# Optimization experiments

Hardware: AMD Instinct MI355X
Metric: run time of the kernel (lower is better)

The kernel has to match this reference:

```python
import jax, jax.numpy as jnp
import numpy as np

B, T = 512, 64
STOCH, DETER, HIDDEN = 30, 200, 200
A, EMBED = 12, 1024
MIN_STD = 0.1
UPDATE_BIAS = -1.0


def _linear_init(key, fan_in, fan_out):
    w_key, b_key = jax.random.split(key)
    lim = 1.0 / np.sqrt(fan_in)
    W = jax.random.uniform(w_key, (fan_in, fan_out), minval=-lim, maxval=lim, dtype=jnp.float32)
    b = jax.random.uniform(b_key, (fan_out,), minval=-lim, maxval=lim, dtype=jnp.float32)
    return W, b


def setup_inputs() -> dict:
    key = jax.random.key(0)
    ks = jax.random.split(key, 12)
    embed = jax.random.normal(ks[0], (B, T, EMBED), dtype=jnp.float32)
    action = jax.random.normal(ks[1], (B, T, A), dtype=jnp.float32)
    noise_prior = jax.random.normal(ks[2], (B, T, STOCH), dtype=jnp.float32)
    noise_post = jax.random.normal(ks[3], (B, T, STOCH), dtype=jnp.float32)
    inp_W, inp_b = _linear_init(ks[4], STOCH + A, HIDDEN)          # _inp_layers
    gru_W, gru_b = _linear_init(ks[5], HIDDEN + DETER, 3 * DETER)  # GRUCell._layer
    img_out_W, img_out_b = _linear_init(ks[6], DETER, HIDDEN)      # _img_out_layers
    ims_W, ims_b = _linear_init(ks[7], HIDDEN, 2 * STOCH)          # _ims_stat_layer
    obs_out_W, obs_out_b = _linear_init(ks[8], DETER + EMBED, HIDDEN)  # _obs_out_layers
    obs_W, obs_b = _linear_init(ks[9], HIDDEN, 2 * STOCH)          # _obs_stat_layer
    return dict(embed=embed, action=action, noise_prior=noise_prior, noise_post=noise_post,
                inp_W=inp_W, inp_b=inp_b, gru_W=gru_W, gru_b=gru_b,
                img_out_W=img_out_W, img_out_b=img_out_b, ims_W=ims_W, ims_b=ims_b,
                obs_out_W=obs_out_W, obs_out_b=obs_out_b, obs_W=obs_W, obs_b=obs_b)


def _observe(embed, action, noise_prior, noise_post,
             inp_W, inp_b, gru_W, gru_b, img_out_W, img_out_b,
             ims_W, ims_b, obs_out_W, obs_out_b, obs_W, obs_b):
    # time-major for scan: [T, B, ...]
    emb_t = jnp.swapaxes(embed, 0, 1)
    act_t = jnp.swapaxes(action, 0, 1)
    npr_t = jnp.swapaxes(noise_prior, 0, 1)
    npo_t = jnp.swapaxes(noise_post, 0, 1)

    def step(carry, xs):
        stoch, deter = carry                    # posterior stoch [B,STOCH], deter [B,DETER]
        a, e, nz_pr, nz_po = xs
        # img_step: input MLP
        x = jax.nn.elu(jnp.concatenate([stoch, a], -1) @ inp_W + inp_b)
        # GRUCell (norm=False)
        parts = jnp.concatenate([x, deter], -1) @ gru_W + gru_b   # [B, 3*DETER]
        reset, cand, update = jnp.split(parts, 3, -1)
        reset = jax.nn.sigmoid(reset)
        cand = jnp.tanh(reset * cand)
        update = jax.nn.sigmoid(update + UPDATE_BIAS)
        deter_new = update * cand + (1.0 - update) * deter
        # prior stats
        h = jax.nn.elu(deter_new @ img_out_W + img_out_b)
        mean_pr, std_pr = jnp.split(h @ ims_W + ims_b, 2, -1)
        std_pr = jax.nn.softplus(std_pr) + MIN_STD
        stoch_pr = mean_pr + std_pr * nz_pr
        # posterior (temp_post=True): cat(deter, embed)
        ho = jax.nn.elu(jnp.concatenate([deter_new, e], -1) @ obs_out_W + obs_out_b)
        mean_po, std_po = jnp.split(ho @ obs_W + obs_b, 2, -1)
        std_po = jax.nn.softplus(std_po) + MIN_STD
        stoch_po = mean_po + std_po * nz_po
        out = (stoch_po, mean_po, std_po, stoch_pr, mean_pr, std_pr, deter_new)
        return (stoch_po, deter_new), out

    init = (jnp.zeros((B, STOCH), jnp.float32), jnp.zeros((B, DETER), jnp.float32))
    _, outs = jax.lax.scan(step, init, (act_t, emb_t, npr_t, npo_t))
    # back to batch-major and pack into a single array [B, T, 6*STOCH + DETER]
    outs = [jnp.swapaxes(o, 0, 1) for o in outs]
    return jnp.concatenate(outs, -1)


def reference(embed, action, noise_prior, noise_post,
              inp_W, inp_b, gru_W, gru_b, img_out_W, img_out_b,
              ims_W, ims_b, obs_out_W, obs_out_b, obs_W, obs_b):
    return _observe(embed, action, noise_prior, noise_post,
                    inp_W, inp_b, gru_W, gru_b, img_out_W, img_out_b,
                    ims_W, ims_b, obs_out_W, obs_out_b, obs_W, obs_b)
```

## Files before the change

### kernel.cpp

```cpp
#include <hip/hip_runtime.h>

typedef _Float16 h2   __attribute__((ext_vector_type(2)));
typedef _Float16 h4   __attribute__((ext_vector_type(4)));
typedef _Float16 half8 __attribute__((ext_vector_type(8)));
typedef float f32x4   __attribute__((ext_vector_type(4)));

#define MFMA16(a,b,c) __builtin_amdgcn_mfma_f32_16x16x32_f16((a),(b),(c),0,0,0)
#define ATOMIC_ST(p,v) __hip_atomic_store((p),(v),__ATOMIC_RELAXED,__HIP_MEMORY_SCOPE_AGENT)
#define ATOMIC_LD(p)   __hip_atomic_load((p),__ATOMIC_RELAXED,__HIP_MEMORY_SCOPE_AGENT)


#define EP_HALVES ((size_t)32768*208)

__global__ void prep_frags(const float* __restrict__ inpW, const float* __restrict__ gruW,
                           const float* __restrict__ imgW, const float* __restrict__ obsoutW,
                           const float* __restrict__ imsW, const float* __restrict__ obsW,
                           _Float16* __restrict__ frags) {
    int gb = blockIdx.x, lane = threadIdx.x;
    const float* src; int KS, K, N, ld, roff = 0, local;
    if (gb < 26)       { src = inpW;    KS = 2;  K = 42;   N = 200; ld = 200; local = gb; }
    else if (gb < 520) { src = gruW;    KS = 13; K = 400;  N = 600; ld = 600; local = gb - 26; }
    else if (gb < 611) { src = imgW;    KS = 7;  K = 200;  N = 200; ld = 200; local = gb - 520; }
    else if (gb < 702) { src = obsoutW; KS = 7;  K = 200;  N = 200; ld = 200; local = gb - 611; }
    else if (gb < 730) { src = imsW;    KS = 7;  K = 200;  N = 60;  ld = 60;  local = gb - 702; }
    else if (gb < 758) { src = obsW;    KS = 7;  K = 200;  N = 60;  ld = 60;  local = gb - 730; }
    else               { src = obsoutW; KS = 32; K = 1024; N = 200; ld = 200; roff = 200; local = gb - 758; }
    int nt = local / KS, ks = local % KS;
    int n  = nt * 16 + (lane & 15);
    int k0 = ks * 32 + (lane >> 4) * 8;
    half8 v;
#pragma unroll
    for (int j = 0; j < 8; ++j) {
        int k = k0 + j;
        float f = (k < K && n < N) ? src[(size_t)(k + roff) * ld + n] : 0.0f;
        v[j] = (_Float16)f;
    }
    *(half8*)(frags + (size_t)gb * 512 + lane * 8) = v;
}

__global__ __launch_bounds__(256) void ep_gemm(const float* __restrict__ embed,
                                               const _Float16* __restrict__ w2f,
                                               _Float16* __restrict__ ep) {
    __shared__ __align__(16) _Float16 aE[16 * 1048];
    int tid = threadIdx.x;
    int rb = blockIdx.x * 16;
#pragma unroll
    for (int i = 0; i < 16; ++i) {
        float4 e = *((const float4*)(embed + (size_t)(rb + i) * 1024) + tid);
        h4 hv; hv[0] = (_Float16)e.x; hv[1] = (_Float16)e.y; hv[2] = (_Float16)e.z; hv[3] = (_Float16)e.w;
        *(h4*)(aE + i * 1048 + tid * 4) = hv;
    }
    __syncthreads();
    int w = tid >> 6, lane = tid & 63, m = lane & 15, q = lane >> 4;
    f32x4 acc[4] = {};
    int nts[4]; int ntc = 0;
    for (int nt = w; nt < 13; nt += 4) nts[ntc++] = nt;
    half8 bb[2][4];
#pragma unroll
    for (int j = 0; j < 4; ++j) if (j < ntc)
        bb[0][j] = *(const half8*)(w2f + ((size_t)(nts[j] * 32) * 64 + lane) * 8);
#pragma unroll
    for (int ks = 0; ks < 32; ++ks) {
        int cur = ks & 1, nxt = cur ^ 1;
        if (ks < 31) {
#pragma unroll
            for (int j = 0; j < 4; ++j) if (j < ntc)
                bb[nxt][j] = *(const half8*)(w2f + ((size_t)(nts[j] * 32 + ks + 1) * 64 + lane) * 8);
        }
        half8 a = *(const half8*)(aE + m * 1048 + ks * 32 + q * 8);
#pragma unroll
        for (int j = 0; j < 4; ++j) if (j < ntc)
            acc[j] = MFMA16(a, bb[cur][j], acc[j]);
    }
    for (int j = 0; j < ntc; ++j) {
        int col = nts[j] * 16 + m;
#pragma unroll
        for (int i = 0; i < 4; ++i)
            ep[(size_t)(rb + q * 4 + i) * 208 + col] = (_Float16)acc[j][i];
    }
}

__device__ __forceinline__ float sigm_(float x) { return 1.0f / (1.0f + __expf(-x)); }
__device__ __forceinline__ float tanh_(float x) { float e = __expf(2.0f * x); return 1.0f - 2.0f / (e + 1.0f); }
__device__ __forceinline__ float elu_(float x)  { return x > 0.0f ? x : __expf(x) - 1.0f; }
__device__ __forceinline__ float sp_(float x)   { return fmaxf(x, 0.0f) + log1pf(__expf(-fabsf(x))); }
__device__ __forceinline__ unsigned packh2(float a, float b) {
    h2 p; p[0] = (_Float16)a; p[1] = (_Float16)b;
    return __builtin_bit_cast(unsigned, p);
}

__global__ __launch_bounds__(512, 2) void rssm_scan(
    const float* __restrict__ action, const float* __restrict__ npr, const float* __restrict__ npo,
    const float* __restrict__ inp_b, const float* __restrict__ gru_b,
    const float* __restrict__ img_b, const float* __restrict__ obsout_b,
    const float* __restrict__ ims_b, const float* __restrict__ obs_b,
    const _Float16* __restrict__ frags, const _Float16* __restrict__ ep,
    unsigned* __restrict__ qdet, unsigned* __restrict__ stochb,
    unsigned* __restrict__ flags, float* __restrict__ out) {

    __shared__ __align__(16) unsigned actI[16 * 36];
    __shared__ __align__(16) unsigned actG[16 * 212];
    __shared__ __align__(16) unsigned actX[16 * 116];
    __shared__ __align__(16) _Float16 parts[16 * 208];
    __shared__ float statspre[16 * 65];
    __shared__ float bias[1320];

    const _Float16* Finp  = frags;
    const _Float16* Fgru  = frags + (size_t)26  * 512;
    const _Float16* Fimg  = frags + (size_t)520 * 512;
    const _Float16* Fobsd = frags + (size_t)611 * 512;
    const _Float16* Fims  = frags + (size_t)702 * 512;
    const _Float16* Fobs  = frags + (size_t)730 * 512;

    const int tid = threadIdx.x, w = tid >> 6, lane = tid & 63, m = lane & 15, q = lane >> 4;
    const int g = blockIdx.x & 31, wg = blockIdx.x >> 5;
    const int rb = g * 16;
    const bool post = (wg >= 2);
    const bool statside = (wg == 0) || (wg == 2);
    unsigned* gf = flags + g * 512;

    for (int i = tid; i < 1320; i += 512) {
        float v;
        if (i < 200) v = inp_b[i];
        else if (i < 800)  v = gru_b[i - 200];
        else if (i < 1000) v = img_b[i - 800];
        else if (i < 1200) v = obsout_b[i - 1000];
        else if (i < 1260) v = ims_b[i - 1200];
        else               v = obs_b[i - 1260];
        bias[i] = v;
    }
    for (int i = tid; i < 16 * 36;  i += 512) actI[i] = 0u;
    for (int i = tid; i < 16 * 212; i += 512) actG[i] = 0u;
    for (int i = tid; i < 16 * 116; i += 512) actX[i] = 0u;

    half8 bgru0[13];
    {
        int tA = (w < 4) ? (3 * wg + w) : (12 + 3 * wg + (w - 4));
#pragma unroll
        for (int ks = 0; ks < 13; ++ks)
            bgru0[ks] = *(const half8*)(Fgru + ((size_t)(tA * 13 + ks) * 64 + lane) * 8);
    }
    half8 bgru1[13];
    if (w < 4) {
        int tB = 25 + 3 * wg + w;
#pragma unroll
        for (int ks = 0; ks < 13; ++ks)
            bgru1[ks] = *(const half8*)(Fgru + ((size_t)(tB * 13 + ks) * 64 + lane) * 8);
    }
    const _Float16* F3 = post ? Fobsd : Fimg;
    const _Float16* F4 = post ? Fobs : Fims;
    half8 bp3a[7];
    if (statside) {
#pragma unroll
        for (int ks = 0; ks < 7; ++ks)
            bp3a[ks] = *(const half8*)(F3 + ((size_t)(w * 7 + ks) * 64 + lane) * 8);
    }
    half8 bp4[7];
    if (statside && w >= 4) {
#pragma unroll
        for (int ks = 0; ks < 7; ++ks)
            bp4[ks] = *(const half8*)(F4 + ((size_t)((w - 4) * 7 + ks) * 64 + lane) * 8);
    }
    __syncthreads();

    for (int t = 0; t < 64; ++t) {
        if (t > 0 && wg != 2) {
            if (tid == 0) {
                unsigned* f = gf + (t - 1) * 8 + 4;
                int it = 0;
                while (ATOMIC_LD(f) != (unsigned)t) {
                    __builtin_amdgcn_s_sleep(1);
                    if (++it > (1 << 20)) break;
                }
            }
            __syncthreads();
            __atomic_signal_fence(__ATOMIC_ACQUIRE);
            if (tid < 240) {
                int r = tid / 15, cp = tid % 15;
                actI[r * 36 + cp] =
                    ATOMIC_LD(stochb + (size_t)((((t - 1) & 1) * 32 + g)) * 256 + r * 16 + cp);
            }
        }
        if (tid < 96) {
            int r = tid / 6, cp = tid % 6;
            float2 a2 = *(const float2*)(action + ((size_t)(rb + r) * 64 + t) * 12 + 2 * cp);
            actI[r * 36 + 15 + cp] = packh2(a2.x, a2.y);
        }
        float2 nz = make_float2(0.0f, 0.0f);
        if (statside && tid < 240) {
            int r = tid / 15, cp = tid % 15;
            const float* ns = post ? npo : npr;
            nz = *(const float2*)(ns + ((size_t)(rb + r) * 64 + t) * 30 + 2 * cp);
        }
        __syncthreads();

        {
            half8 bi0[2], bi1[2];
#pragma unroll
            for (int ks = 0; ks < 2; ++ks)
                bi0[ks] = *(const half8*)(Finp + ((size_t)(w * 2 + ks) * 64 + lane) * 8);
            if (w < 5) {
#pragma unroll
                for (int ks = 0; ks < 2; ++ks)
                    bi1[ks] = *(const half8*)(Finp + ((size_t)((8 + w) * 2 + ks) * 64 + lane) * 8);
            }
            f32x4 acc = {}, acc2 = {};
#pragma unroll
            for (int ks = 0; ks < 2; ++ks) {
                half8 a = *(const half8*)(actI + m * 36 + ks * 16 + q * 4);
                acc = MFMA16(a, bi0[ks], acc);
                if (w < 5) acc2 = MFMA16(a, bi1[ks], acc2);
            }
            f32x4 accN;
#pragma unroll
            for (int i = 0; i < 4; ++i) accN[i] = __shfl_xor(acc[i], 1);
            if (!(m & 1)) {
                int col = w * 16 + m;
#pragma unroll
                for (int i = 0; i < 4; ++i)
                    actG[(q * 4 + i) * 212 + (col >> 1)] =
                        packh2(elu_(acc[i] + bias[col]), elu_(accN[i] + bias[col + 1]));
            }
            if (w < 5) {
                f32x4 acc2N;
#pragma unroll
                for (int i = 0; i < 4; ++i) acc2N[i] = __shfl_xor(acc2[i], 1);
                if (!(m & 1)) {
                    int col = (8 + w) * 16 + m;
                    if (col < 200) {
#pragma unroll
                        for (int i = 0; i < 4; ++i)
                            actG[(q * 4 + i) * 212 + (col >> 1)] =
                                packh2(elu_(acc2[i] + bias[col]), elu_(acc2N[i] + bias[col + 1]));
                    }
                }
            }
        }
        __syncthreads();

        {
            f32x4 a0 = {}, a1 = {};
#pragma unroll
            for (int ks = 0; ks < 13; ++ks) {
                half8 a = *(const half8*)(actG + m * 212 + ks * 16 + q * 4);
                a0 = MFMA16(a, bgru0[ks], a0);
                if (w < 4) a1 = MFMA16(a, bgru1[ks], a1);
            }
#pragma unroll
            for (int i = 0; i < 4; ++i)
                parts[(q * 4 + i) * 208 + w * 16 + m] = (_Float16)a0[i];
            if (w < 4) {
#pragma unroll
                for (int i = 0; i < 4; ++i)
                    parts[(q * 4 + i) * 208 + (8 + w) * 16 + m] = (_Float16)a1[i];
            }
        }
        half8 pf3[7];
        if (statside && w < 5) {
#pragma unroll
            for (int ks = 0; ks < 7; ++ks)
                pf3[ks] = *(const half8*)(F3 + ((size_t)((8 + w) * 7 + ks) * 64 + lane) * 8);
        }
        __syncthreads();

        unsigned* qd = qdet + (size_t)((t & 1) * 32 + g) * 1600;
        if (tid < 400) {
            int r = tid / 25, p = tid % 25;
            int n0 = 50 * wg + 2 * p;
            float pg[3][2];
#pragma unroll
            for (int j = 0; j < 3; ++j) {
                int cg = n0 + 200 * j;
                int bj = (j == 0) ? 3 * wg : (j == 1) ? 12 + 3 * wg : 25 + 3 * wg;
                int lt = 4 * j + (cg >> 4) - bj;
                h2 v = *(const h2*)(parts + r * 208 + lt * 16 + (cg & 15));
                pg[j][0] = (float)v[0] + bias[200 + cg];
                pg[j][1] = (float)v[1] + bias[200 + cg + 1];
            }
            h2 dold = *(const h2*)&actG[r * 212 + 100 + (n0 >> 1)];
            float dn[2];
#pragma unroll
            for (int e = 0; e < 2; ++e) {
                float reset = sigm_(pg[0][e]);
                float cand  = tanh_(reset * pg[1][e]);
                float upd   = sigm_(pg[2][e] - 1.0f);
                dn[e] = upd * cand + (1.0f - upd) * (float)dold[e];
            }
            unsigned pk = packh2(dn[0], dn[1]);
            actG[r * 212 + 100 + (n0 >> 1)] = pk;
            ATOMIC_ST(qd + r * 100 + (n0 >> 1), pk);
            *(float2*)(out + ((size_t)(rb + r) * 64 + t) * 380 + 180 + n0) = make_float2(dn[0], dn[1]);
        }
        __syncthreads();

        __atomic_signal_fence(__ATOMIC_RELEASE);
        if (tid == 0) ATOMIC_ST(gf + t * 8 + wg, (unsigned)(t + 1));
        if (tid < 3) {
            unsigned* f = gf + t * 8 + ((wg + 1 + tid) & 3);
            int it = 0;
            while (ATOMIC_LD(f) != (unsigned)(t + 1)) {
                __builtin_amdgcn_s_sleep(1);
                if (++it > (1 << 20)) break;
            }
        }
        __syncthreads();
        __atomic_signal_fence(__ATOMIC_ACQUIRE);
        for (int i = tid; i < 1200; i += 512) {
            int r = i / 75, idx = i % 75;
            int pp = (25 * (wg + 1) + idx) % 100;
            actG[r * 212 + 100 + pp] = ATOMIC_LD(qd + r * 100 + pp);
        }
        __syncthreads();

        if (statside) {
            int colA = w * 16 + m;
            int colB = (8 + w) * 16 + m;
            h2 epA[4], epB[4];
            if (post && !(m & 1)) {
#pragma unroll
                for (int i = 0; i < 4; ++i)
                    epA[i] = *(const h2*)(ep + ((size_t)(rb + q * 4 + i) * 64 + t) * 208 + colA);
                if (w < 5 && colB < 200) {
#pragma unroll
                    for (int i = 0; i < 4; ++i)
                        epB[i] = *(const h2*)(ep + ((size_t)(rb + q * 4 + i) * 64 + t) * 208 + colB);
                }
            }
            f32x4 acc = {}, acc2 = {};
#pragma unroll
            for (int ks = 0; ks < 7; ++ks) {
                half8 a = *(const half8*)(actG + m * 212 + 100 + ks * 16 + q * 4);
                acc = MFMA16(a, bp3a[ks], acc);
                if (w < 5) acc2 = MFMA16(a, pf3[ks], acc2);
            }
            f32x4 accN;
#pragma unroll
            for (int i = 0; i < 4; ++i) accN[i] = __shfl_xor(acc[i], 1);
            if (!(m & 1)) {
                int bb0 = post ? 1000 : 800;
#pragma unroll
                for (int i = 0; i < 4; ++i) {
                    float e0 = post ? (float)epA[i][0] : 0.0f;
                    float e1 = post ? (float)epA[i][1] : 0.0f;
                    actX[(q * 4 + i) * 116 + (colA >> 1)] =
                        packh2(elu_(acc[i] + bias[bb0 + colA] + e0),
                               elu_(accN[i] + bias[bb0 + colA + 1] + e1));
                }
            }
            if (w < 5) {
                f32x4 acc2N;
#pragma unroll
                for (int i = 0; i < 4; ++i) acc2N[i] = __shfl_xor(acc2[i], 1);
                if (!(m & 1) && colB < 200) {
                    int bb0 = post ? 1000 : 800;
#pragma unroll
                    for (int i = 0; i < 4; ++i) {
                        float e0 = post ? (float)epB[i][0] : 0.0f;
                        float e1 = post ? (float)epB[i][1] : 0.0f;
                        actX[(q * 4 + i) * 116 + (colB >> 1)] =
                            packh2(elu_(acc2[i] + bias[bb0 + colB] + e0),
                                   elu_(acc2N[i] + bias[bb0 + colB + 1] + e1));
                    }
                }
            }
        }
        __syncthreads();

        if (statside && w >= 4) {
            f32x4 acc = {};
#pragma unroll
            for (int ks = 0; ks < 7; ++ks) {
                half8 a = *(const half8*)(actX + m * 116 + ks * 16 + q * 4);
                acc = MFMA16(a, bp4[ks], acc);
            }
#pragma unroll
            for (int i = 0; i < 4; ++i)
                statspre[(q * 4 + i) * 65 + (w - 4) * 16 + m] = acc[i];
        }
        __syncthreads();

        if (statside && tid < 240) {
            int r = tid / 15, cp = tid % 15;
            int bb0 = post ? 1260 : 1200;
            float m0 = statspre[r * 65 + 2 * cp]     + bias[bb0 + 2 * cp];
            float m1 = statspre[r * 65 + 2 * cp + 1] + bias[bb0 + 2 * cp + 1];
            float s0 = sp_(statspre[r * 65 + 30 + 2 * cp]     + bias[bb0 + 30 + 2 * cp]) + 0.1f;
            float s1 = sp_(statspre[r * 65 + 30 + 2 * cp + 1] + bias[bb0 + 30 + 2 * cp + 1]) + 0.1f;
            float st0 = m0 + s0 * nz.x, st1 = m1 + s1 * nz.y;
            size_t ob = ((size_t)(rb + r) * 64 + t) * 380;
            int o0 = post ? 0 : 90;
            *(float2*)(out + ob + o0 + 2 * cp)      = make_float2(st0, st1);
            *(float2*)(out + ob + o0 + 30 + 2 * cp) = make_float2(m0, m1);
            *(float2*)(out + ob + o0 + 60 + 2 * cp) = make_float2(s0, s1);
            if (post) {
                unsigned pk = packh2(st0, st1);
                actI[r * 36 + cp] = pk;
                ATOMIC_ST(stochb + (size_t)((t & 1) * 32 + g) * 256 + r * 16 + cp, pk);
            }
        }
        __syncthreads();
        if (wg == 2 && t < 63) {
            __atomic_signal_fence(__ATOMIC_RELEASE);
            if (tid == 0) ATOMIC_ST(gf + t * 8 + 4, (unsigned)(t + 1));
        }
    }
}

extern "C" void kernel_launch(void* const* d_in, const int* in_sizes, int n_in,
                              void* d_out, int out_size, void* d_ws, size_t ws_size,
                              hipStream_t stream) {
    const float* embed   = (const float*)d_in[0];
    const float* action  = (const float*)d_in[1];
    const float* npr     = (const float*)d_in[2];
    const float* npo     = (const float*)d_in[3];
    const float* inpW    = (const float*)d_in[4];
    const float* inpb    = (const float*)d_in[5];
    const float* gruW    = (const float*)d_in[6];
    const float* grub    = (const float*)d_in[7];
    const float* imgW    = (const float*)d_in[8];
    const float* imgb    = (const float*)d_in[9];
    const float* imsW    = (const float*)d_in[10];
    const float* imsb    = (const float*)d_in[11];
    const float* obsoutW = (const float*)d_in[12];
    const float* obsoutb = (const float*)d_in[13];
    const float* obsW    = (const float*)d_in[14];
    const float* obsb    = (const float*)d_in[15];

    char* ws = (char*)d_ws;
    _Float16* ep     = (_Float16*)ws;
    _Float16* frags  = (_Float16*)(ws + EP_HALVES * 2);
    char* p          = ws + EP_HALVES * 2 + (size_t)1174 * 1024;
    unsigned* qdetb  = (unsigned*)p;
    p += (size_t)2 * 32 * 1600 * 4;
    unsigned* stochb = (unsigned*)p;
    p += (size_t)2 * 32 * 256 * 4;
    unsigned* flags  = (unsigned*)p;

    prep_frags<<<1174, 64, 0, stream>>>(inpW, gruW, imgW, obsoutW, imsW, obsW, frags);
    ep_gemm<<<2048, 256, 0, stream>>>(embed, frags + (size_t)758 * 512, ep);
    rssm_scan<<<128, 512, 0, stream>>>(action, npr, npo, inpb, grub, imgb, obsoutb,
                                       imsb, obsb, frags, ep, qdetb, stochb, flags,
                                       (float*)d_out);
}
```

Baseline: 999.1 us.

## Use LDS-only barriers, hoist weight/embed loads, and defer output stores past flag release

Most __syncthreads are replaced with a barrier that waits only on LDS counters (lgkmcnt), so outstanding global stores and loads no longer stall each step barrier. The input-layer weight fragments move out of the time loop into registers. The per-step embed-projection loads are issued at the top of the step to overlap with the flag wait. Global output stores are moved after the cross-block flag release so they stay off the critical inter-block dependency path. In exchange, register pressure rises, and correctness now relies on global loads being consumed only after their own waits.

```diff
diff --git a/kernel.cpp b/kernel.cpp
--- a/kernel.cpp
+++ b/kernel.cpp
@@ -8,6 +8,9 @@
 #define MFMA16(a,b,c) __builtin_amdgcn_mfma_f32_16x16x32_f16((a),(b),(c),0,0,0)
 #define ATOMIC_ST(p,v) __hip_atomic_store((p),(v),__ATOMIC_RELAXED,__HIP_MEMORY_SCOPE_AGENT)
 #define ATOMIC_LD(p)   __hip_atomic_load((p),__ATOMIC_RELAXED,__HIP_MEMORY_SCOPE_AGENT)
+#define BAR_LDS() do { asm volatile("s_waitcnt lgkmcnt(0)" ::: "memory"); \
+                       __builtin_amdgcn_s_barrier();                      \
+                       asm volatile("" ::: "memory"); } while (0)
 
 
 #define EP_HALVES ((size_t)32768*208)
@@ -89,7 +92,7 @@
     return __builtin_bit_cast(unsigned, p);
 }
 
-__global__ __launch_bounds__(512, 2) void rssm_scan(
+__global__ __launch_bounds__(512) __attribute__((amdgpu_waves_per_eu(2, 2))) void rssm_scan(
     const float* __restrict__ action, const float* __restrict__ npr, const float* __restrict__ npo,
     const float* __restrict__ inp_b, const float* __restrict__ gru_b,
     const float* __restrict__ img_b, const float* __restrict__ obsout_b,
@@ -117,6 +120,8 @@
     const int rb = g * 16;
     const bool post = (wg >= 2);
     const bool statside = (wg == 0) || (wg == 2);
+    const int colA = w * 16 + m;
+    const int colB = (8 + w) * 16 + m;
     unsigned* gf = flags + g * 512;
 
     for (int i = tid; i < 1320; i += 512) {
@@ -147,6 +152,15 @@
         for (int ks = 0; ks < 13; ++ks)
             bgru1[ks] = *(const half8*)(Fgru + ((size_t)(tB * 13 + ks) * 64 + lane) * 8);
     }
+    half8 bi0[2], bi1[2];
+#pragma unroll
+    for (int ks = 0; ks < 2; ++ks)
+        bi0[ks] = *(const half8*)(Finp + ((size_t)(w * 2 + ks) * 64 + lane) * 8);
+    if (w < 5) {
+#pragma unroll
+        for (int ks = 0; ks < 2; ++ks)
+            bi1[ks] = *(const half8*)(Finp + ((size_t)((8 + w) * 2 + ks) * 64 + lane) * 8);
+    }
     const _Float16* F3 = post ? Fobsd : Fimg;
     const _Float16* F4 = post ? Fobs : Fims;
     half8 bp3a[7];
@@ -164,6 +178,18 @@
     __syncthreads();
 
     for (int t = 0; t < 64; ++t) {
+        h2 epA[4], epB[4];
+        if (post && !(m & 1)) {
+#pragma unroll
+            for (int i = 0; i < 4; ++i)
+                epA[i] = *(const h2*)(ep + ((size_t)(rb + q * 4 + i) * 64 + t) * 208 + colA);
+            if (w < 5 && colB < 200) {
+#pragma unroll
+                for (int i = 0; i < 4; ++i)
+                    epB[i] = *(const h2*)(ep + ((size_t)(rb + q * 4 + i) * 64 + t) * 208 + colB);
+            }
+        }
+
         if (t > 0 && wg != 2) {
             if (tid == 0) {
                 unsigned* f = gf + (t - 1) * 8 + 4;
@@ -173,7 +199,7 @@
                     if (++it > (1 << 20)) break;
                 }
             }
-            __syncthreads();
+            BAR_LDS();
             __atomic_signal_fence(__ATOMIC_ACQUIRE);
             if (tid < 240) {
                 int r = tid / 15, cp = tid % 15;
@@ -192,18 +218,9 @@
             const float* ns = post ? npo : npr;
             nz = *(const float2*)(ns + ((size_t)(rb + r) * 64 + t) * 30 + 2 * cp);
         }
-        __syncthreads();
+        BAR_LDS();
 
         {
-            half8 bi0[2], bi1[2];
-#pragma unroll
-            for (int ks = 0; ks < 2; ++ks)
-                bi0[ks] = *(const half8*)(Finp + ((size_t)(w * 2 + ks) * 64 + lane) * 8);
-            if (w < 5) {
-#pragma unroll
-                for (int ks = 0; ks < 2; ++ks)
-                    bi1[ks] = *(const half8*)(Finp + ((size_t)((8 + w) * 2 + ks) * 64 + lane) * 8);
-            }
             f32x4 acc = {}, acc2 = {};
 #pragma unroll
             for (int ks = 0; ks < 2; ++ks) {
@@ -236,7 +253,7 @@
                 }
             }
         }
-        __syncthreads();
+        BAR_LDS();
 
         {
             f32x4 a0 = {}, a1 = {};
@@ -261,9 +278,10 @@
             for (int ks = 0; ks < 7; ++ks)
                 pf3[ks] = *(const half8*)(F3 + ((size_t)((8 + w) * 7 + ks) * 64 + lane) * 8);
         }
-        __syncthreads();
+        BAR_LDS();
 
         unsigned* qd = qdet + (size_t)((t & 1) * 32 + g) * 1600;
+        float gdn0 = 0.0f, gdn1 = 0.0f; int gr = 0, gn0 = 0;
         if (tid < 400) {
             int r = tid / 25, p = tid % 25;
             int n0 = 50 * wg + 2 * p;
@@ -289,12 +307,14 @@
             unsigned pk = packh2(dn[0], dn[1]);
             actG[r * 212 + 100 + (n0 >> 1)] = pk;
             ATOMIC_ST(qd + r * 100 + (n0 >> 1), pk);
-            *(float2*)(out + ((size_t)(rb + r) * 64 + t) * 380 + 180 + n0) = make_float2(dn[0], dn[1]);
+            gdn0 = dn[0]; gdn1 = dn[1]; gr = r; gn0 = n0;
         }
         __syncthreads();
 
         __atomic_signal_fence(__ATOMIC_RELEASE);
         if (tid == 0) ATOMIC_ST(gf + t * 8 + wg, (unsigned)(t + 1));
+        if (tid < 400)
+            *(float2*)(out + ((size_t)(rb + gr) * 64 + t) * 380 + 180 + gn0) = make_float2(gdn0, gdn1);
         if (tid < 3) {
             unsigned* f = gf + t * 8 + ((wg + 1 + tid) & 3);
             int it = 0;
@@ -303,29 +323,16 @@
                 if (++it > (1 << 20)) break;
             }
         }
-        __syncthreads();
+        BAR_LDS();
         __atomic_signal_fence(__ATOMIC_ACQUIRE);
         for (int i = tid; i < 1200; i += 512) {
             int r = i / 75, idx = i % 75;
             int pp = (25 * (wg + 1) + idx) % 100;
             actG[r * 212 + 100 + pp] = ATOMIC_LD(qd + r * 100 + pp);
         }
-        __syncthreads();
+        BAR_LDS();
 
         if (statside) {
-            int colA = w * 16 + m;
-            int colB = (8 + w) * 16 + m;
-            h2 epA[4], epB[4];
-            if (post && !(m & 1)) {
-#pragma unroll
-                for (int i = 0; i < 4; ++i)
-                    epA[i] = *(const h2*)(ep + ((size_t)(rb + q * 4 + i) * 64 + t) * 208 + colA);
-                if (w < 5 && colB < 200) {
-#pragma unroll
-                    for (int i = 0; i < 4; ++i)
-                        epB[i] = *(const h2*)(ep + ((size_t)(rb + q * 4 + i) * 64 + t) * 208 + colB);
-                }
-            }
             f32x4 acc = {}, acc2 = {};
 #pragma unroll
             for (int ks = 0; ks < 7; ++ks) {
@@ -364,7 +371,7 @@
                 }
             }
         }
-        __syncthreads();
+        BAR_LDS();
 
         if (statside && w >= 4) {
             f32x4 acc = {};
@@ -377,8 +384,10 @@
             for (int i = 0; i < 4; ++i)
                 statspre[(q * 4 + i) * 65 + (w - 4) * 16 + m] = acc[i];
         }
-        __syncthreads();
-
+        BAR_LDS();
+
+        float o0v = 0.f, o1v = 0.f, o2v = 0.f, o3v = 0.f, o4v = 0.f, o5v = 0.f;
+        int pr = 0, pcp = 0; bool doout = false;
         if (statside && tid < 240) {
             int r = tid / 15, cp = tid % 15;
             int bb0 = post ? 1260 : 1200;
@@ -387,21 +396,25 @@
             float s0 = sp_(statspre[r * 65 + 30 + 2 * cp]     + bias[bb0 + 30 + 2 * cp]) + 0.1f;
             float s1 = sp_(statspre[r * 65 + 30 + 2 * cp + 1] + bias[bb0 + 30 + 2 * cp + 1]) + 0.1f;
             float st0 = m0 + s0 * nz.x, st1 = m1 + s1 * nz.y;
-            size_t ob = ((size_t)(rb + r) * 64 + t) * 380;
-            int o0 = post ? 0 : 90;
-            *(float2*)(out + ob + o0 + 2 * cp)      = make_float2(st0, st1);
-            *(float2*)(out + ob + o0 + 30 + 2 * cp) = make_float2(m0, m1);
-            *(float2*)(out + ob + o0 + 60 + 2 * cp) = make_float2(s0, s1);
             if (post) {
                 unsigned pk = packh2(st0, st1);
                 actI[r * 36 + cp] = pk;
                 ATOMIC_ST(stochb + (size_t)((t & 1) * 32 + g) * 256 + r * 16 + cp, pk);
             }
+            o0v = st0; o1v = st1; o2v = m0; o3v = m1; o4v = s0; o5v = s1;
+            pr = r; pcp = cp; doout = true;
         }
         __syncthreads();
         if (wg == 2 && t < 63) {
             __atomic_signal_fence(__ATOMIC_RELEASE);
             if (tid == 0) ATOMIC_ST(gf + t * 8 + 4, (unsigned)(t + 1));
+        }
+        if (doout) {
+            size_t ob = ((size_t)(rb + pr) * 64 + t) * 380;
+            int o0 = post ? 0 : 90;
+            *(float2*)(out + ob + o0 + 2 * pcp)      = make_float2(o0v, o1v);
+            *(float2*)(out + ob + o0 + 30 + 2 * pcp) = make_float2(o2v, o3v);
+            *(float2*)(out + ob + o0 + 60 + 2 * pcp) = make_float2(o4v, o5v);
         }
     }
 }
```

After: 948.8 us. 1.05x faster.
